# Kernel optimization log

Hardware: AMD Instinct MI355X
Metric: run time of the kernel (lower is better)

Reference implementation:

```python
import jax, jax.numpy as jnp
import numpy as np

# SLAYER neuron / simulation hyperparameters (from network.yaml)
THETA = 10.0      # spike threshold
TAU_SR = 10.0     # SRM (PSP) kernel time constant [ms]
TAU_REF = 1.0     # refractory kernel time constant [ms]
SCALE_REF = 2.0   # refractory kernel scale
TS = 1.0          # simulation step [ms]
K_SRM = 100       # truncation length of SRM kernel (eps decays ~0 by 10*tau)
K_REF = 32        # truncation length of refractory kernel (tauRef=1 -> decays fast)


def _eps_kernel(tau, k):
    # eps(t) = (t/tau) * exp(1 - t/tau), eps(0) = 0  (SLAYER SRM alpha kernel)
    t = jnp.arange(k, dtype=jnp.float32) * TS
    return (t / tau) * jnp.exp(1.0 - t / tau)


def psp(x, kern):
    # Causal temporal filter: y[..., t] = sum_j kern[j] * x[..., t - j]
    B, N, T = x.shape
    lhs = x.reshape(B * N, 1, T)
    rhs = kern[::-1].reshape(1, 1, -1)  # lax.conv is cross-correlation -> flip
    y = jax.lax.conv_general_dilated(
        lhs, rhs, window_strides=(1,), padding=[(kern.shape[0] - 1, 0)],
        dimension_numbers=('NCH', 'OIH', 'NCH'))
    return y.reshape(B, N, T)


def spike(u, refk):
    # Sequential thresholding with refractory feedback (SLAYER spikeFunction fwd).
    # u: [B, N, T] membrane drive. State r: future refractory contributions.
    kr = refk.shape[0]
    refk_shift = jnp.concatenate([refk[1:], jnp.zeros((1,), refk.dtype)])

    def step(r, u_t):
        m = u_t + r[..., 0]                      # membrane potential at t
        s = (m >= THETA).astype(u_t.dtype)       # hard spike
        r_next = jnp.concatenate([r[..., 1:], jnp.zeros_like(r[..., :1])], -1) \
                 + s[..., None] * refk_shift     # add refractory response
        return r_next, s

    uT = jnp.moveaxis(u, -1, 0)                  # [T, B, N]
    r0 = jnp.zeros(uT.shape[1:] + (kr,), u.dtype)
    _, sT = jax.lax.scan(step, r0, uT)
    return jnp.moveaxis(sT, 0, -1) / TS          # [B, N, T]


def setup_inputs() -> dict:
    key = jax.random.key(0)
    k1, k2, k3 = jax.random.split(key, 3)
    B, NIN, NHID, NOUT, T = 32, 2048, 512, 10, 350
    spike_input = (jax.random.uniform(k1, (B, NIN, T)) < 0.05).astype(jnp.float32)
    W1 = jax.random.normal(k2, (NHID, NIN), dtype=jnp.float32) * 0.05
    W2 = jax.random.normal(k3, (NOUT, NHID), dtype=jnp.float32) * 0.05
    return {"spike_input": spike_input, "W1": W1, "W2": W2}


def reference(spike_input, W1, W2):
    srm = _eps_kernel(TAU_SR, K_SRM)
    refk = -SCALE_REF * THETA * _eps_kernel(TAU_REF, K_REF)
    # layer 1: psp -> dense -> spike
    a1 = jnp.einsum('bnt,mn->bmt', psp(spike_input, srm), W1)
    s1 = spike(a1, refk)
    # layer 2: psp -> dense -> spike
    a2 = jnp.einsum('bnt,mn->bmt', psp(s1, srm), W2)
    s2 = spike(a2, refk)
    return s2
```

## Files before the change

kernel.cpp:

```cpp
#include <hip/hip_runtime.h>
#include <stdint.h>

static constexpr int B  = 32;
static constexpr int T  = 350;
static constexpr int NIN = 2048;
static constexpr int NH  = 512;
static constexpr int NO  = 10;
static constexpr int BT  = B * T;

static constexpr float THETA = 10.0f;
static constexpr float BETA  = 0.36787944117144233f;
static constexpr float CREF  = 54.365636569180904707f;

static constexpr size_t OFF_W1TS = 0;
static constexpr size_t OFF_MASK = 4196352;
static constexpr size_t OFF_SRM  = 7080960;
static constexpr size_t OFF_Z1   = 7081984;
static constexpr size_t OFF_A1   = 30019584;
static constexpr size_t OFF_LST  = OFF_A1;
static constexpr size_t OFF_CNT  = OFF_A1 + 4300800;
static constexpr size_t OFF_SMK  = 52957184;

static constexpr int SLICE_F = 8;
static constexpr int NSLICE  = NH / SLICE_F;
static constexpr int SLICE_STRIDE = 2049 * SLICE_F;

__global__ void __launch_bounds__(256) k_prep(const float* __restrict__ x,
                                              const float* __restrict__ W1,
                                              float* __restrict__ W1Ts,
                                              uint64_t* __restrict__ mask,
                                              float* __restrict__ srm28) {
    int bid = blockIdx.x;
    if (bid < 1024) {
        __shared__ uint64_t tb[6][64];
        int b = bid >> 5, nblk = bid & 31;
        int wv = threadIdx.x >> 6, lane = threadIdx.x & 63;
        for (int g = 0; g < 4; ++g) {
            float v[4][6];
            #pragma unroll
            for (int i = 0; i < 4; ++i) {
                int nr = wv + 4 * (4 * g + i);
                const float* xp = x + ((size_t)b * NIN + nblk * 64 + nr) * T;
                #pragma unroll
                for (int c = 0; c < 6; ++c) {
                    int t = c * 64 + lane;
                    v[i][c] = (t < T) ? xp[t] : 0.f;
                }
            }
            #pragma unroll
            for (int i = 0; i < 4; ++i) {
                int nr = wv + 4 * (4 * g + i);
                #pragma unroll
                for (int c = 0; c < 6; ++c) {
                    uint64_t mk = __ballot(v[i][c] != 0.0f);
                    if (lane == 0) tb[c][nr] = mk;
                }
            }
        }
        __syncthreads();
        static const uint64_t AM[6] = {
            0x00000000FFFFFFFFull, 0x0000FFFF0000FFFFull, 0x00FF00FF00FF00FFull,
            0x0F0F0F0F0F0F0F0Full, 0x3333333333333333ull, 0x5555555555555555ull };
        for (int c = wv; c < 6; c += 4) {
            uint64_t w = tb[c][lane];
            #pragma unroll
            for (int i = 0; i < 6; ++i) {
                int s = 32 >> i;
                uint64_t A = AM[i];
                uint64_t y = __shfl_xor((unsigned long long)w, s);
                if ((lane & s) == 0) w = (w & A)  | ((y & A) << s);
                else                 w = (w & ~A) | ((y & ~A) >> s);
            }
            int t = c * 64 + lane;
            if (t < T) mask[((size_t)b * 32 + nblk) * 352 + t] = w;
        }
    } else if (bid < 2048) {
        __shared__ float tile[32][33];
        int idx = bid - 1024;
        int n0 = (idx & 63) * 32, m0 = (idx >> 6) * 32;
        int tx = threadIdx.x & 31, ty0 = threadIdx.x >> 5;
        #pragma unroll
        for (int i = 0; i < 4; ++i) {
            int ty = ty0 + 8 * i;
            tile[ty][tx] = W1[(size_t)(m0 + ty) * NIN + n0 + tx];
        }
        __syncthreads();
        #pragma unroll
        for (int i = 0; i < 4; ++i) {
            int ty = ty0 + 8 * i;
            int n = n0 + ty, m = m0 + tx;
            W1Ts[(size_t)(m >> 3) * SLICE_STRIDE + n * SLICE_F + (m & 7)] = tile[tx][ty];
        }
    } else {
        int j = threadIdx.x;
        if (j < 192) {
            float v = 0.f;
            int i = j - 28;
            if (i >= 0 && i < 100) { float t = (float)i; v = (t * 0.1f) * expf(1.f - t * 0.1f); }
            srm28[j] = v;
        }
        for (int i = j; i < NSLICE * SLICE_F; i += 256)
            W1Ts[(size_t)(i >> 3) * SLICE_STRIDE + 2048 * SLICE_F + (i & 7)] = 0.f;
    }
}

__global__ void __launch_bounds__(64) k_decode(const uint64_t* __restrict__ mask,
                                               uint16_t* __restrict__ glst,
                                               int* __restrict__ gcnt) {
    __shared__ uint16_t lst[192];
    int t = blockIdx.x, b = blockIdx.y;
    int row = b * T + t;
    int lane = threadIdx.x;
    uint64_t w = (lane < 32) ? mask[((size_t)b * 32 + lane) * 352 + t] : 0ull;
    int cnt = __popcll(w);
    int pre = cnt;
    #pragma unroll
    for (int off = 1; off < 64; off <<= 1) {
        int v = __shfl_up(pre, off);
        if (lane >= off) pre += v;
    }
    int total = __shfl(pre, 63);
    int excl = pre - cnt;
    while (w) {
        int bit = __builtin_ctzll(w);
        w &= w - 1;
        lst[excl++] = (uint16_t)((lane << 6) + bit);
    }
    int padded = (total + 7) & ~7;
    if (lane < padded - total) lst[total + lane] = 2048;
    __syncthreads();
    uint16_t* op = glst + (size_t)row * 192;
    for (int i = lane; i < padded; i += 64) op[i] = lst[i];
    if (lane == 0) gcnt[row] = padded;
}

__global__ void __launch_bounds__(256) k_z1s(const uint16_t* __restrict__ glst,
                                             const int* __restrict__ gcnt,
                                             const float* __restrict__ W1Ts,
                                             float* __restrict__ z1) {
    __shared__ float w1s[SLICE_STRIDE];
    int s = blockIdx.x;
    int bt0 = blockIdx.y * (BT / 8);
    const float4* src = (const float4*)(W1Ts + (size_t)s * SLICE_STRIDE);
    for (int i = threadIdx.x; i < SLICE_STRIDE / 4; i += 256)
        ((float4*)w1s)[i] = src[i];
    __syncthreads();

    int q  = threadIdx.x & 1;
    int rl = threadIdx.x >> 1;
    for (int rr = rl; rr < BT / 8; rr += 128) {
        int row = bt0 + rr;
        int padded = gcnt[row];
        const ushort4* lp = (const ushort4*)(glst + (size_t)row * 192);
        float4 acc = {0, 0, 0, 0};
        for (int k = 0; k < padded; k += 8) {
            ushort4 q0 = lp[k >> 2];
            ushort4 q1 = lp[(k >> 2) + 1];
            const float* base = w1s + q * 4;
            float4 x0 = *(const float4*)(base + q0.x * SLICE_F);
            float4 x1 = *(const float4*)(base + q0.y * SLICE_F);
            float4 x2 = *(const float4*)(base + q0.z * SLICE_F);
            float4 x3 = *(const float4*)(base + q0.w * SLICE_F);
            float4 x4 = *(const float4*)(base + q1.x * SLICE_F);
            float4 x5 = *(const float4*)(base + q1.y * SLICE_F);
            float4 x6 = *(const float4*)(base + q1.z * SLICE_F);
            float4 x7 = *(const float4*)(base + q1.w * SLICE_F);
            acc.x += x0.x; acc.y += x0.y; acc.z += x0.z; acc.w += x0.w;
            acc.x += x1.x; acc.y += x1.y; acc.z += x1.z; acc.w += x1.w;
            acc.x += x2.x; acc.y += x2.y; acc.z += x2.z; acc.w += x2.w;
            acc.x += x3.x; acc.y += x3.y; acc.z += x3.z; acc.w += x3.w;
            acc.x += x4.x; acc.y += x4.y; acc.z += x4.z; acc.w += x4.w;
            acc.x += x5.x; acc.y += x5.y; acc.z += x5.z; acc.w += x5.w;
            acc.x += x6.x; acc.y += x6.y; acc.z += x6.z; acc.w += x6.w;
            acc.x += x7.x; acc.y += x7.y; acc.z += x7.z; acc.w += x7.w;
        }
        *(float4*)(z1 + (size_t)row * NH + s * SLICE_F + q * 4) = acc;
    }
}

__global__ void __launch_bounds__(64) k_fir1(const float* __restrict__ src,
                                             float* __restrict__ dst,
                                             const float* __restrict__ srm28) {
    __shared__ float tb[192];
    int b = blockIdx.x, half = blockIdx.y, tg = blockIdx.z;
    int lane = threadIdx.x;
    for (int i = lane; i < 192; i += 64) tb[i] = srm28[i];
    __syncthreads();
    int t0 = tg * 16;
    int m = half * 256 + lane * 4;
    const float* sp = src + (size_t)b * T * NH + m;

    float4 acc[16];
    #pragma unroll
    for (int r = 0; r < 16; ++r) acc[r] = make_float4(0.f, 0.f, 0.f, 0.f);

    int o_start = (99 - t0) >> 4;
    if (o_start < 0) o_start = 0;

    for (int o = o_start; o < 7; ++o) {
        float cw[31];
        int cb = 112 - 16 * o;
        #pragma unroll
        for (int k = 0; k < 31; ++k) cw[k] = tb[cb + k];
        int dd0 = o * 16;
        #pragma unroll
        for (int j = 0; j < 16; ++j) {
            int tau = t0 - 99 + dd0 + j;
            float4 v = make_float4(0.f, 0.f, 0.f, 0.f);
            if (tau >= 0 && tau < T) v = *(const float4*)(sp + (size_t)tau * NH);
            #pragma unroll
            for (int r = 0; r < 16; ++r) {
                float c = cw[r - j + 15];
                acc[r].x += c * v.x; acc[r].y += c * v.y;
                acc[r].z += c * v.z; acc[r].w += c * v.w;
            }
        }
    }
    {
        float e1 = tb[29], e2 = tb[30];
        int tau = t0 + 13;
        if (tau < T) {
            float4 v = *(const float4*)(sp + (size_t)tau * NH);
            acc[14].x += e1 * v.x; acc[14].y += e1 * v.y;
            acc[14].z += e1 * v.z; acc[14].w += e1 * v.w;
            acc[15].x += e2 * v.x; acc[15].y += e2 * v.y;
            acc[15].z += e2 * v.z; acc[15].w += e2 * v.w;
        }
        tau = t0 + 14;
        if (tau < T) {
            float4 v = *(const float4*)(sp + (size_t)tau * NH);
            acc[15].x += e1 * v.x; acc[15].y += e1 * v.y;
            acc[15].z += e1 * v.z; acc[15].w += e1 * v.w;
        }
    }
    #pragma unroll
    for (int r = 0; r < 16; ++r) {
        int t = t0 + r;
        if (t < T) *(float4*)(dst + ((size_t)b * T + t) * NH + m) = acc[r];
    }
}

__global__ void __launch_bounds__(64) k_scan1(const float* __restrict__ a1,
                                              uint64_t* __restrict__ smaskg) {
    constexpr int CT = 16;
    constexpr int NC = (T + CT - 1) / CT;
    int tid = blockIdx.x * 64 + threadIdx.x;
    int b = tid >> 9, m = tid & 511;
    int w8 = m >> 6;
    const float* up = a1 + (size_t)b * T * NH + m;
    float A = 0.f, Bs = 0.f;
    float c0[CT], c1[CT], c2[CT];
    #pragma unroll
    for (int j = 0; j < CT; ++j) c0[j] = up[(size_t)j * NH];
    #pragma unroll
    for (int j = 0; j < CT; ++j) {
        int t = CT + j;
        c1[j] = (t < T) ? up[(size_t)t * NH] : 0.f;
    }
    for (int c = 0; c < NC; ++c) {
        int t0 = c * CT;
        int nsteps = (T - t0 < CT) ? (T - t0) : CT;
        if (c + 2 < NC) {
            #pragma unroll
            for (int j = 0; j < CT; ++j) {
                int t = t0 + 2 * CT + j;
                c2[j] = (t < T) ? up[(size_t)t * NH] : 0.f;
            }
        }
        #pragma unroll
        for (int j = 0; j < CT; ++j) {
            if (j < nsteps) {
                float mem = c0[j] - CREF * Bs;
                float sp = (mem >= THETA) ? 1.0f : 0.0f;
                A = sp + BETA * A;
                Bs = BETA * (Bs + A);
                uint64_t mk = __ballot(sp != 0.0f);
                if (threadIdx.x == 0) smaskg[((size_t)b * T + t0 + j) * 8 + w8] = mk;
            }
        }
        #pragma unroll
        for (int j = 0; j < CT; ++j) { c0[j] = c1[j]; c1[j] = c2[j]; }
    }
}

__global__ void __launch_bounds__(256) k_tail(const uint64_t* __restrict__ smaskg,
                                              const float* __restrict__ W2,
                                              const float* __restrict__ srm28,
                                              float* __restrict__ out) {
    __shared__ float w2s_ab[NO * NH];
    __shared__ uint64_t smk[T * 8];
    __shared__ float tb[192];
    __shared__ float zb[350 * 11 + 16];
    int b = blockIdx.x, tid = threadIdx.x;
    for (int i = tid; i < NO * NH; i += 256) w2s_ab[i] = W2[i];
    const uint64_t* mp = smaskg + (size_t)b * T * 8;
    for (int i = tid; i < T * 8; i += 256) smk[i] = mp[i];
    if (tid < 192) tb[tid] = srm28[tid];
    __syncthreads();
    for (int i = tid; i < T * NO; i += 256) {
        int t = i / NO, o = i - t * NO;
        const float* wrow = w2s_ab + o * NH;
        float acc = 0.f;
        #pragma unroll
        for (int w8 = 0; w8 < 8; ++w8) {
            uint64_t mk = smk[t * 8 + w8];
            int base = w8 * 64;
            while (mk) {
                int bit = __builtin_ctzll(mk);
                mk &= mk - 1;
                acc += wrow[base + bit];
            }
        }
        zb[t * 11 + o] = acc;
    }
    __syncthreads();
    float* ab = w2s_ab;
    if (tid < 220) {
        int tt = tid / 10, o = tid - tt * 10;
        int t0 = tt * 16;
        float acc[16];
        #pragma unroll
        for (int r = 0; r < 16; ++r) acc[r] = 0.f;
        float c[16];
        #pragma unroll
        for (int r = 0; r < 16; ++r) c[r] = tb[r + 127];
        for (int oo = 0; oo < 8; ++oo) {
            #pragma unroll
            for (int j = 0; j < 16; ++j) {
                int dd = oo * 16 + j;
                int tau = t0 - 99 + dd;
                float v = (tau >= 0 && tau < T) ? zb[tau * 11 + o] : 0.f;
                #pragma unroll
                for (int r = 0; r < 16; ++r) acc[r] += c[r] * v;
                #pragma unroll
                for (int r = 15; r > 0; --r) c[r] = c[r - 1];
                int ci = 126 - dd;
                c[0] = tb[ci < 0 ? 0 : ci];
            }
        }
        #pragma unroll
        for (int r = 0; r < 16; ++r) {
            int t = t0 + r;
            if (t < T) ab[t * 10 + o] = acc[r];
        }
    }
    __syncthreads();
    if (tid < NO) {
        int o = tid;
        float A2 = 0.f, B2 = 0.f;
        float* op = out + ((size_t)b * NO + o) * T;
        for (int t = 0; t < T; ++t) {
            float mem = ab[t * 10 + o] - CREF * B2;
            float sp = (mem >= THETA) ? 1.0f : 0.0f;
            A2 = sp + BETA * A2;
            B2 = BETA * (B2 + A2);
            op[t] = sp;
        }
    }
}

extern "C" void kernel_launch(void* const* d_in, const int* in_sizes, int n_in,
                              void* d_out, int out_size, void* d_ws, size_t ws_size,
                              hipStream_t stream) {
    const float* x  = (const float*)d_in[0];
    const float* W1 = (const float*)d_in[1];
    const float* W2 = (const float*)d_in[2];
    char* ws = (char*)d_ws;
    float*    W1Ts   = (float*)(ws + OFF_W1TS);
    uint64_t* mask   = (uint64_t*)(ws + OFF_MASK);
    float*    srm    = (float*)(ws + OFF_SRM);
    float*    z1     = (float*)(ws + OFF_Z1);
    float*    a1     = (float*)(ws + OFF_A1);
    uint16_t* glst   = (uint16_t*)(ws + OFF_LST);
    int*      gcnt   = (int*)(ws + OFF_CNT);
    uint64_t* smaskg = (uint64_t*)(ws + OFF_SMK);
    float*    out    = (float*)d_out;

    hipLaunchKernelGGL(k_prep,   dim3(2049),      dim3(256), 0, stream, x, W1, W1Ts, mask, srm);
    hipLaunchKernelGGL(k_decode, dim3(T, B),      dim3(64),  0, stream, mask, glst, gcnt);
    hipLaunchKernelGGL(k_z1s,    dim3(NSLICE, 8), dim3(256), 0, stream, glst, gcnt, W1Ts, z1);
    hipLaunchKernelGGL(k_fir1,   dim3(B, 2, 22),  dim3(64),  0, stream, z1, a1, srm);
    hipLaunchKernelGGL(k_scan1,  dim3(256),       dim3(64),  0, stream, a1, smaskg);
    hipLaunchKernelGGL(k_tail,   dim3(B),         dim3(256), 0, stream, smaskg, W2, srm, out);
}
```

Baseline: 294.6 us.

## Fuse all stages into one persistent kernel with grid-wide atomic barriers

The six separate kernel launches become a single persistent kernel of 512 blocks. Each stage loops over its former virtual blocks and is separated from the next by a software grid barrier built on atomic counters, which are zeroed with a memset before launch. The goal is to remove per-launch overhead and the gaps between kernels. In exchange, occupancy is fixed at 2 blocks per CU, a 64KB shared buffer limits residency, stages with little parallelism such as the tail (32 blocks) leave most of the grid idle, and the barrier deadlocks if the 512 blocks cannot all be resident at once.

```diff
diff --git a/kernel.cpp b/kernel.cpp
--- a/kernel.cpp
+++ b/kernel.cpp
@@ -7,6 +7,8 @@
 static constexpr int NH  = 512;
 static constexpr int NO  = 10;
 static constexpr int BT  = B * T;
+
+static constexpr int GRID = 512;
 
 static constexpr float THETA = 10.0f;
 static constexpr float BETA  = 0.36787944117144233f;
@@ -20,341 +22,379 @@
 static constexpr size_t OFF_LST  = OFF_A1;
 static constexpr size_t OFF_CNT  = OFF_A1 + 4300800;
 static constexpr size_t OFF_SMK  = 52957184;
+static constexpr size_t OFF_BAR  = 53673984;
 
 static constexpr int SLICE_F = 8;
 static constexpr int NSLICE  = NH / SLICE_F;
 static constexpr int SLICE_STRIDE = 2049 * SLICE_F;
 
-__global__ void __launch_bounds__(256) k_prep(const float* __restrict__ x,
-                                              const float* __restrict__ W1,
-                                              float* __restrict__ W1Ts,
-                                              uint64_t* __restrict__ mask,
-                                              float* __restrict__ srm28) {
+__device__ __forceinline__ void gbar(int* cnt, int idx) {
+    __syncthreads();
+    __threadfence();
+    if (threadIdx.x == 0) {
+        atomicAdd(cnt + idx, 1);
+        while (__hip_atomic_load(cnt + idx, __ATOMIC_ACQUIRE,
+                                 __HIP_MEMORY_SCOPE_AGENT) < GRID) {
+            __builtin_amdgcn_s_sleep(1);
+        }
+    }
+    __syncthreads();
+    __threadfence();
+}
+
+__global__ void __launch_bounds__(256, 2) k_all(const float* __restrict__ x,
+                                                const float* __restrict__ W1,
+                                                const float* __restrict__ W2,
+                                                float* __restrict__ W1Ts,
+                                                uint64_t* __restrict__ mask,
+                                                float* __restrict__ srm28,
+                                                uint16_t* glst,
+                                                int* __restrict__ gcnt,
+                                                float* __restrict__ z1,
+                                                float* a1,
+                                                uint64_t* __restrict__ smaskg,
+                                                int* __restrict__ bar,
+                                                float* __restrict__ out) {
+    __shared__ __align__(16) char smem[65568];
     int bid = blockIdx.x;
-    if (bid < 1024) {
-        __shared__ uint64_t tb[6][64];
-        int b = bid >> 5, nblk = bid & 31;
-        int wv = threadIdx.x >> 6, lane = threadIdx.x & 63;
-        for (int g = 0; g < 4; ++g) {
-            float v[4][6];
+    int tid = threadIdx.x;
+
+    for (int vb = bid; vb < 2049; vb += GRID) {
+        if (vb < 1024) {
+            uint64_t (*tb)[64] = (uint64_t(*)[64])smem;
+            int b = vb >> 5, nblk = vb & 31;
+            int wv = tid >> 6, lane = tid & 63;
+            for (int g = 0; g < 4; ++g) {
+                float v[4][6];
+                #pragma unroll
+                for (int i = 0; i < 4; ++i) {
+                    int nr = wv + 4 * (4 * g + i);
+                    const float* xp = x + ((size_t)b * NIN + nblk * 64 + nr) * T;
+                    #pragma unroll
+                    for (int c = 0; c < 6; ++c) {
+                        int t = c * 64 + lane;
+                        v[i][c] = (t < T) ? xp[t] : 0.f;
+                    }
+                }
+                #pragma unroll
+                for (int i = 0; i < 4; ++i) {
+                    int nr = wv + 4 * (4 * g + i);
+                    #pragma unroll
+                    for (int c = 0; c < 6; ++c) {
+                        uint64_t mk = __ballot(v[i][c] != 0.0f);
+                        if (lane == 0) tb[c][nr] = mk;
+                    }
+                }
+            }
+            __syncthreads();
+            static const uint64_t AM[6] = {
+                0x00000000FFFFFFFFull, 0x0000FFFF0000FFFFull, 0x00FF00FF00FF00FFull,
+                0x0F0F0F0F0F0F0F0Full, 0x3333333333333333ull, 0x5555555555555555ull };
+            for (int c = wv; c < 6; c += 4) {
+                uint64_t w = tb[c][lane];
+                #pragma unroll
+                for (int i = 0; i < 6; ++i) {
+                    int s = 32 >> i;
+                    uint64_t A = AM[i];
+                    uint64_t y = __shfl_xor((unsigned long long)w, s);
+                    if ((lane & s) == 0) w = (w & A)  | ((y & A) << s);
+                    else                 w = (w & ~A) | ((y & ~A) >> s);
+                }
+                int t = c * 64 + lane;
+                if (t < T) mask[((size_t)b * 32 + nblk) * 352 + t] = w;
+            }
+        } else if (vb < 2048) {
+            float (*tile)[33] = (float(*)[33])smem;
+            int idx = vb - 1024;
+            int n0 = (idx & 63) * 32, m0 = (idx >> 6) * 32;
+            int tx = tid & 31, ty0 = tid >> 5;
             #pragma unroll
             for (int i = 0; i < 4; ++i) {
-                int nr = wv + 4 * (4 * g + i);
-                const float* xp = x + ((size_t)b * NIN + nblk * 64 + nr) * T;
-                #pragma unroll
-                for (int c = 0; c < 6; ++c) {
-                    int t = c * 64 + lane;
-                    v[i][c] = (t < T) ? xp[t] : 0.f;
-                }
-            }
+                int ty = ty0 + 8 * i;
+                tile[ty][tx] = W1[(size_t)(m0 + ty) * NIN + n0 + tx];
+            }
+            __syncthreads();
             #pragma unroll
             for (int i = 0; i < 4; ++i) {
-                int nr = wv + 4 * (4 * g + i);
-                #pragma unroll
-                for (int c = 0; c < 6; ++c) {
-                    uint64_t mk = __ballot(v[i][c] != 0.0f);
-                    if (lane == 0) tb[c][nr] = mk;
-                }
-            }
-        }
-        __syncthreads();
-        static const uint64_t AM[6] = {
-            0x00000000FFFFFFFFull, 0x0000FFFF0000FFFFull, 0x00FF00FF00FF00FFull,
-            0x0F0F0F0F0F0F0F0Full, 0x3333333333333333ull, 0x5555555555555555ull };
-        for (int c = wv; c < 6; c += 4) {
-            uint64_t w = tb[c][lane];
-            #pragma unroll
-            for (int i = 0; i < 6; ++i) {
-                int s = 32 >> i;
-                uint64_t A = AM[i];
-                uint64_t y = __shfl_xor((unsigned long long)w, s);
-                if ((lane & s) == 0) w = (w & A)  | ((y & A) << s);
-                else                 w = (w & ~A) | ((y & ~A) >> s);
-            }
-            int t = c * 64 + lane;
-            if (t < T) mask[((size_t)b * 32 + nblk) * 352 + t] = w;
-        }
-    } else if (bid < 2048) {
-        __shared__ float tile[32][33];
-        int idx = bid - 1024;
-        int n0 = (idx & 63) * 32, m0 = (idx >> 6) * 32;
-        int tx = threadIdx.x & 31, ty0 = threadIdx.x >> 5;
-        #pragma unroll
-        for (int i = 0; i < 4; ++i) {
-            int ty = ty0 + 8 * i;
-            tile[ty][tx] = W1[(size_t)(m0 + ty) * NIN + n0 + tx];
-        }
-        __syncthreads();
-        #pragma unroll
-        for (int i = 0; i < 4; ++i) {
-            int ty = ty0 + 8 * i;
-            int n = n0 + ty, m = m0 + tx;
-            W1Ts[(size_t)(m >> 3) * SLICE_STRIDE + n * SLICE_F + (m & 7)] = tile[tx][ty];
-        }
-    } else {
-        int j = threadIdx.x;
-        if (j < 192) {
-            float v = 0.f;
-            int i = j - 28;
-            if (i >= 0 && i < 100) { float t = (float)i; v = (t * 0.1f) * expf(1.f - t * 0.1f); }
-            srm28[j] = v;
-        }
-        for (int i = j; i < NSLICE * SLICE_F; i += 256)
-            W1Ts[(size_t)(i >> 3) * SLICE_STRIDE + 2048 * SLICE_F + (i & 7)] = 0.f;
-    }
-}
-
-__global__ void __launch_bounds__(64) k_decode(const uint64_t* __restrict__ mask,
-                                               uint16_t* __restrict__ glst,
-                                               int* __restrict__ gcnt) {
-    __shared__ uint16_t lst[192];
-    int t = blockIdx.x, b = blockIdx.y;
-    int row = b * T + t;
-    int lane = threadIdx.x;
-    uint64_t w = (lane < 32) ? mask[((size_t)b * 32 + lane) * 352 + t] : 0ull;
-    int cnt = __popcll(w);
-    int pre = cnt;
-    #pragma unroll
-    for (int off = 1; off < 64; off <<= 1) {
-        int v = __shfl_up(pre, off);
-        if (lane >= off) pre += v;
-    }
-    int total = __shfl(pre, 63);
-    int excl = pre - cnt;
-    while (w) {
-        int bit = __builtin_ctzll(w);
-        w &= w - 1;
-        lst[excl++] = (uint16_t)((lane << 6) + bit);
-    }
-    int padded = (total + 7) & ~7;
-    if (lane < padded - total) lst[total + lane] = 2048;
-    __syncthreads();
-    uint16_t* op = glst + (size_t)row * 192;
-    for (int i = lane; i < padded; i += 64) op[i] = lst[i];
-    if (lane == 0) gcnt[row] = padded;
-}
-
-__global__ void __launch_bounds__(256) k_z1s(const uint16_t* __restrict__ glst,
-                                             const int* __restrict__ gcnt,
-                                             const float* __restrict__ W1Ts,
-                                             float* __restrict__ z1) {
-    __shared__ float w1s[SLICE_STRIDE];
-    int s = blockIdx.x;
-    int bt0 = blockIdx.y * (BT / 8);
-    const float4* src = (const float4*)(W1Ts + (size_t)s * SLICE_STRIDE);
-    for (int i = threadIdx.x; i < SLICE_STRIDE / 4; i += 256)
-        ((float4*)w1s)[i] = src[i];
-    __syncthreads();
-
-    int q  = threadIdx.x & 1;
-    int rl = threadIdx.x >> 1;
-    for (int rr = rl; rr < BT / 8; rr += 128) {
-        int row = bt0 + rr;
-        int padded = gcnt[row];
-        const ushort4* lp = (const ushort4*)(glst + (size_t)row * 192);
-        float4 acc = {0, 0, 0, 0};
-        for (int k = 0; k < padded; k += 8) {
-            ushort4 q0 = lp[k >> 2];
-            ushort4 q1 = lp[(k >> 2) + 1];
-            const float* base = w1s + q * 4;
-            float4 x0 = *(const float4*)(base + q0.x * SLICE_F);
-            float4 x1 = *(const float4*)(base + q0.y * SLICE_F);
-            float4 x2 = *(const float4*)(base + q0.z * SLICE_F);
-            float4 x3 = *(const float4*)(base + q0.w * SLICE_F);
-            float4 x4 = *(const float4*)(base + q1.x * SLICE_F);
-            float4 x5 = *(const float4*)(base + q1.y * SLICE_F);
-            float4 x6 = *(const float4*)(base + q1.z * SLICE_F);
-            float4 x7 = *(const float4*)(base + q1.w * SLICE_F);
-            acc.x += x0.x; acc.y += x0.y; acc.z += x0.z; acc.w += x0.w;
-            acc.x += x1.x; acc.y += x1.y; acc.z += x1.z; acc.w += x1.w;
-            acc.x += x2.x; acc.y += x2.y; acc.z += x2.z; acc.w += x2.w;
-            acc.x += x3.x; acc.y += x3.y; acc.z += x3.z; acc.w += x3.w;
-            acc.x += x4.x; acc.y += x4.y; acc.z += x4.z; acc.w += x4.w;
-            acc.x += x5.x; acc.y += x5.y; acc.z += x5.z; acc.w += x5.w;
-            acc.x += x6.x; acc.y += x6.y; acc.z += x6.z; acc.w += x6.w;
-            acc.x += x7.x; acc.y += x7.y; acc.z += x7.z; acc.w += x7.w;
-        }
-        *(float4*)(z1 + (size_t)row * NH + s * SLICE_F + q * 4) = acc;
-    }
-}
-
-__global__ void __launch_bounds__(64) k_fir1(const float* __restrict__ src,
-                                             float* __restrict__ dst,
-                                             const float* __restrict__ srm28) {
-    __shared__ float tb[192];
-    int b = blockIdx.x, half = blockIdx.y, tg = blockIdx.z;
-    int lane = threadIdx.x;
-    for (int i = lane; i < 192; i += 64) tb[i] = srm28[i];
-    __syncthreads();
-    int t0 = tg * 16;
-    int m = half * 256 + lane * 4;
-    const float* sp = src + (size_t)b * T * NH + m;
-
-    float4 acc[16];
-    #pragma unroll
-    for (int r = 0; r < 16; ++r) acc[r] = make_float4(0.f, 0.f, 0.f, 0.f);
-
-    int o_start = (99 - t0) >> 4;
-    if (o_start < 0) o_start = 0;
-
-    for (int o = o_start; o < 7; ++o) {
-        float cw[31];
-        int cb = 112 - 16 * o;
-        #pragma unroll
-        for (int k = 0; k < 31; ++k) cw[k] = tb[cb + k];
-        int dd0 = o * 16;
-        #pragma unroll
-        for (int j = 0; j < 16; ++j) {
-            int tau = t0 - 99 + dd0 + j;
-            float4 v = make_float4(0.f, 0.f, 0.f, 0.f);
-            if (tau >= 0 && tau < T) v = *(const float4*)(sp + (size_t)tau * NH);
+                int ty = ty0 + 8 * i;
+                int n = n0 + ty, m = m0 + tx;
+                W1Ts[(size_t)(m >> 3) * SLICE_STRIDE + n * SLICE_F + (m & 7)] = tile[tx][ty];
+            }
+        } else {
+            int j = tid;
+            if (j < 192) {
+                float v = 0.f;
+                int i = j - 28;
+                if (i >= 0 && i < 100) { float t = (float)i; v = (t * 0.1f) * expf(1.f - t * 0.1f); }
+                srm28[j] = v;
+            }
+            for (int i = j; i < NSLICE * SLICE_F; i += 256)
+                W1Ts[(size_t)(i >> 3) * SLICE_STRIDE + 2048 * SLICE_F + (i & 7)] = 0.f;
+        }
+        __syncthreads();
+    }
+    gbar(bar, 0);
+
+    {
+        int w = tid >> 6, lane = tid & 63;
+        uint16_t* lst = (uint16_t*)smem + w * 200;
+        int vw = bid * 4 + w;
+        for (int k = 0; k < 6; ++k) {
+            int row = vw + 2048 * k;
+            bool act = (row < BT);
+            int padded = 0;
+            if (act) {
+                int b = row / T, t = row - b * T;
+                uint64_t wd = (lane < 32) ? mask[((size_t)b * 32 + lane) * 352 + t] : 0ull;
+                int cnt = __popcll(wd);
+                int pre = cnt;
+                #pragma unroll
+                for (int off = 1; off < 64; off <<= 1) {
+                    int v = __shfl_up(pre, off);
+                    if (lane >= off) pre += v;
+                }
+                int total = __shfl(pre, 63);
+                int excl = pre - cnt;
+                while (wd) {
+                    int bit = __builtin_ctzll(wd);
+                    wd &= wd - 1;
+                    lst[excl++] = (uint16_t)((lane << 6) + bit);
+                }
+                padded = (total + 7) & ~7;
+                if (lane < padded - total) lst[total + lane] = 2048;
+            }
+            __syncthreads();
+            if (act) {
+                uint16_t* op = glst + (size_t)row * 192;
+                for (int i = lane; i < padded; i += 64) op[i] = lst[i];
+                if (lane == 0) gcnt[row] = padded;
+            }
+            __syncthreads();
+        }
+    }
+    gbar(bar, 1);
+
+    {
+        float* w1s = (float*)smem;
+        int s = bid & 63;
+        int bt0 = (bid >> 6) * (BT / 8);
+        const float4* src = (const float4*)(W1Ts + (size_t)s * SLICE_STRIDE);
+        for (int i = tid; i < SLICE_STRIDE / 4; i += 256)
+            ((float4*)w1s)[i] = src[i];
+        __syncthreads();
+
+        int q  = tid & 1;
+        int rl = tid >> 1;
+        for (int rr = rl; rr < BT / 8; rr += 128) {
+            int row = bt0 + rr;
+            int padded = gcnt[row];
+            const ushort4* lp = (const ushort4*)(glst + (size_t)row * 192);
+            float4 acc = {0, 0, 0, 0};
+            for (int k = 0; k < padded; k += 8) {
+                ushort4 q0 = lp[k >> 2];
+                ushort4 q1 = lp[(k >> 2) + 1];
+                const float* base = w1s + q * 4;
+                float4 x0 = *(const float4*)(base + q0.x * SLICE_F);
+                float4 x1 = *(const float4*)(base + q0.y * SLICE_F);
+                float4 x2 = *(const float4*)(base + q0.z * SLICE_F);
+                float4 x3 = *(const float4*)(base + q0.w * SLICE_F);
+                float4 x4 = *(const float4*)(base + q1.x * SLICE_F);
+                float4 x5 = *(const float4*)(base + q1.y * SLICE_F);
+                float4 x6 = *(const float4*)(base + q1.z * SLICE_F);
+                float4 x7 = *(const float4*)(base + q1.w * SLICE_F);
+                acc.x += x0.x; acc.y += x0.y; acc.z += x0.z; acc.w += x0.w;
+                acc.x += x1.x; acc.y += x1.y; acc.z += x1.z; acc.w += x1.w;
+                acc.x += x2.x; acc.y += x2.y; acc.z += x2.z; acc.w += x2.w;
+                acc.x += x3.x; acc.y += x3.y; acc.z += x3.z; acc.w += x3.w;
+                acc.x += x4.x; acc.y += x4.y; acc.z += x4.z; acc.w += x4.w;
+                acc.x += x5.x; acc.y += x5.y; acc.z += x5.z; acc.w += x5.w;
+                acc.x += x6.x; acc.y += x6.y; acc.z += x6.z; acc.w += x6.w;
+                acc.x += x7.x; acc.y += x7.y; acc.z += x7.z; acc.w += x7.w;
+            }
+            *(float4*)(z1 + (size_t)row * NH + s * SLICE_F + q * 4) = acc;
+        }
+    }
+    gbar(bar, 2);
+
+    {
+        float* tbf = (float*)smem;
+        for (int i = tid; i < 192; i += 256) tbf[i] = srm28[i];
+        __syncthreads();
+        int w = tid >> 6, lane = tid & 63;
+        int vw = bid * 4 + w;
+        if (vw < 1408) {
+            int b = vw & 31, half = (vw >> 5) & 1, tg = vw >> 6;
+            int t0 = tg * 16;
+            int m = half * 256 + lane * 4;
+            const float* sp = z1 + (size_t)b * T * NH + m;
+
+            float4 acc[16];
+            #pragma unroll
+            for (int r = 0; r < 16; ++r) acc[r] = make_float4(0.f, 0.f, 0.f, 0.f);
+
+            int o_start = (99 - t0) >> 4;
+            if (o_start < 0) o_start = 0;
+
+            for (int o = o_start; o < 7; ++o) {
+                float cw[31];
+                int cb = 112 - 16 * o;
+                #pragma unroll
+                for (int kk = 0; kk < 31; ++kk) cw[kk] = tbf[cb + kk];
+                int dd0 = o * 16;
+                #pragma unroll
+                for (int j = 0; j < 16; ++j) {
+                    int tau = t0 - 99 + dd0 + j;
+                    float4 v = make_float4(0.f, 0.f, 0.f, 0.f);
+                    if (tau >= 0 && tau < T) v = *(const float4*)(sp + (size_t)tau * NH);
+                    #pragma unroll
+                    for (int r = 0; r < 16; ++r) {
+                        float c = cw[r - j + 15];
+                        acc[r].x += c * v.x; acc[r].y += c * v.y;
+                        acc[r].z += c * v.z; acc[r].w += c * v.w;
+                    }
+                }
+            }
+            {
+                float e1 = tbf[29], e2 = tbf[30];
+                int tau = t0 + 13;
+                if (tau < T) {
+                    float4 v = *(const float4*)(sp + (size_t)tau * NH);
+                    acc[14].x += e1 * v.x; acc[14].y += e1 * v.y;
+                    acc[14].z += e1 * v.z; acc[14].w += e1 * v.w;
+                    acc[15].x += e2 * v.x; acc[15].y += e2 * v.y;
+                    acc[15].z += e2 * v.z; acc[15].w += e2 * v.w;
+                }
+                tau = t0 + 14;
+                if (tau < T) {
+                    float4 v = *(const float4*)(sp + (size_t)tau * NH);
+                    acc[15].x += e1 * v.x; acc[15].y += e1 * v.y;
+                    acc[15].z += e1 * v.z; acc[15].w += e1 * v.w;
+                }
+            }
             #pragma unroll
             for (int r = 0; r < 16; ++r) {
-                float c = cw[r - j + 15];
-                acc[r].x += c * v.x; acc[r].y += c * v.y;
-                acc[r].z += c * v.z; acc[r].w += c * v.w;
-            }
-        }
-    }
+                int t = t0 + r;
+                if (t < T) *(float4*)(a1 + ((size_t)b * T + t) * NH + m) = acc[r];
+            }
+        }
+    }
+    gbar(bar, 3);
+
     {
-        float e1 = tb[29], e2 = tb[30];
-        int tau = t0 + 13;
-        if (tau < T) {
-            float4 v = *(const float4*)(sp + (size_t)tau * NH);
-            acc[14].x += e1 * v.x; acc[14].y += e1 * v.y;
-            acc[14].z += e1 * v.z; acc[14].w += e1 * v.w;
-            acc[15].x += e2 * v.x; acc[15].y += e2 * v.y;
-            acc[15].z += e2 * v.z; acc[15].w += e2 * v.w;
-        }
-        tau = t0 + 14;
-        if (tau < T) {
-            float4 v = *(const float4*)(sp + (size_t)tau * NH);
-            acc[15].x += e1 * v.x; acc[15].y += e1 * v.y;
-            acc[15].z += e1 * v.z; acc[15].w += e1 * v.w;
-        }
-    }
-    #pragma unroll
-    for (int r = 0; r < 16; ++r) {
-        int t = t0 + r;
-        if (t < T) *(float4*)(dst + ((size_t)b * T + t) * NH + m) = acc[r];
-    }
-}
-
-__global__ void __launch_bounds__(64) k_scan1(const float* __restrict__ a1,
-                                              uint64_t* __restrict__ smaskg) {
-    constexpr int CT = 16;
-    constexpr int NC = (T + CT - 1) / CT;
-    int tid = blockIdx.x * 64 + threadIdx.x;
-    int b = tid >> 9, m = tid & 511;
-    int w8 = m >> 6;
-    const float* up = a1 + (size_t)b * T * NH + m;
-    float A = 0.f, Bs = 0.f;
-    float c0[CT], c1[CT], c2[CT];
-    #pragma unroll
-    for (int j = 0; j < CT; ++j) c0[j] = up[(size_t)j * NH];
-    #pragma unroll
-    for (int j = 0; j < CT; ++j) {
-        int t = CT + j;
-        c1[j] = (t < T) ? up[(size_t)t * NH] : 0.f;
-    }
-    for (int c = 0; c < NC; ++c) {
-        int t0 = c * CT;
-        int nsteps = (T - t0 < CT) ? (T - t0) : CT;
-        if (c + 2 < NC) {
+        if ((bid & 1) == 0 && tid < 64) {
+            constexpr int CT = 16;
+            constexpr int NC = (T + CT - 1) / CT;
+            int tg = (bid >> 1) * 64 + tid;
+            int b = tg >> 9, m = tg & 511;
+            int w8 = m >> 6;
+            const float* up = a1 + (size_t)b * T * NH + m;
+            float A = 0.f, Bs = 0.f;
+            float c0[CT], c1[CT], c2[CT];
+            #pragma unroll
+            for (int j = 0; j < CT; ++j) c0[j] = up[(size_t)j * NH];
             #pragma unroll
             for (int j = 0; j < CT; ++j) {
-                int t = t0 + 2 * CT + j;
-                c2[j] = (t < T) ? up[(size_t)t * NH] : 0.f;
-            }
-        }
-        #pragma unroll
-        for (int j = 0; j < CT; ++j) {
-            if (j < nsteps) {
-                float mem = c0[j] - CREF * Bs;
+                int t = CT + j;
+                c1[j] = (t < T) ? up[(size_t)t * NH] : 0.f;
+            }
+            for (int c = 0; c < NC; ++c) {
+                int t0 = c * CT;
+                int nsteps = (T - t0 < CT) ? (T - t0) : CT;
+                if (c + 2 < NC) {
+                    #pragma unroll
+                    for (int j = 0; j < CT; ++j) {
+                        int t = t0 + 2 * CT + j;
+                        c2[j] = (t < T) ? up[(size_t)t * NH] : 0.f;
+                    }
+                }
+                #pragma unroll
+                for (int j = 0; j < CT; ++j) {
+                    if (j < nsteps) {
+                        float mem = c0[j] - CREF * Bs;
+                        float sp = (mem >= THETA) ? 1.0f : 0.0f;
+                        A = sp + BETA * A;
+                        Bs = BETA * (Bs + A);
+                        uint64_t mk = __ballot(sp != 0.0f);
+                        if (tid == 0) smaskg[((size_t)b * T + t0 + j) * 8 + w8] = mk;
+                    }
+                }
+                #pragma unroll
+                for (int j = 0; j < CT; ++j) { c0[j] = c1[j]; c1[j] = c2[j]; }
+            }
+        }
+    }
+    gbar(bar, 4);
+
+    if ((bid & 15) == 0) {
+        int b = bid >> 4;
+        float*    w2s_ab = (float*)smem;
+        uint64_t* smk    = (uint64_t*)(smem + 20480);
+        float*    tbf    = (float*)(smem + 42880);
+        float*    zb     = (float*)(smem + 43648);
+        for (int i = tid; i < NO * NH; i += 256) w2s_ab[i] = W2[i];
+        const uint64_t* mp = smaskg + (size_t)b * T * 8;
+        for (int i = tid; i < T * 8; i += 256) smk[i] = mp[i];
+        if (tid < 192) tbf[tid] = srm28[tid];
+        __syncthreads();
+        for (int i = tid; i < T * NO; i += 256) {
+            int t = i / NO, o = i - t * NO;
+            const float* wrow = w2s_ab + o * NH;
+            float acc = 0.f;
+            #pragma unroll
+            for (int w8 = 0; w8 < 8; ++w8) {
+                uint64_t mk = smk[t * 8 + w8];
+                int base = w8 * 64;
+                while (mk) {
+                    int bit = __builtin_ctzll(mk);
+                    mk &= mk - 1;
+                    acc += wrow[base + bit];
+                }
+            }
+            zb[t * 11 + o] = acc;
+        }
+        __syncthreads();
+        float* ab = w2s_ab;
+        if (tid < 220) {
+            int tt = tid / 10, o = tid - tt * 10;
+            int t0 = tt * 16;
+            float acc[16];
+            #pragma unroll
+            for (int r = 0; r < 16; ++r) acc[r] = 0.f;
+            float c[16];
+            #pragma unroll
+            for (int r = 0; r < 16; ++r) c[r] = tbf[r + 127];
+            for (int oo = 0; oo < 8; ++oo) {
+                #pragma unroll
+                for (int j = 0; j < 16; ++j) {
+                    int dd = oo * 16 + j;
+                    int tau = t0 - 99 + dd;
+                    float v = (tau >= 0 && tau < T) ? zb[tau * 11 + o] : 0.f;
+                    #pragma unroll
+                    for (int r = 0; r < 16; ++r) acc[r] += c[r] * v;
+                    #pragma unroll
+                    for (int r = 15; r > 0; --r) c[r] = c[r - 1];
+                    int ci = 126 - dd;
+                    c[0] = tbf[ci < 0 ? 0 : ci];
+                }
+            }
+            #pragma unroll
+            for (int r = 0; r < 16; ++r) {
+                int t = t0 + r;
+                if (t < T) ab[t * 10 + o] = acc[r];
+            }
+        }
+        __syncthreads();
+        if (tid < NO) {
+            int o = tid;
+            float A2 = 0.f, B2 = 0.f;
+            float* op = out + ((size_t)b * NO + o) * T;
+            for (int t = 0; t < T; ++t) {
+                float mem = ab[t * 10 + o] - CREF * B2;
                 float sp = (mem >= THETA) ? 1.0f : 0.0f;
-                A = sp + BETA * A;
-                Bs = BETA * (Bs + A);
-                uint64_t mk = __ballot(sp != 0.0f);
-                if (threadIdx.x == 0) smaskg[((size_t)b * T + t0 + j) * 8 + w8] = mk;
-            }
-        }
-        #pragma unroll
-        for (int j = 0; j < CT; ++j) { c0[j] = c1[j]; c1[j] = c2[j]; }
-    }
-}
-
-__global__ void __launch_bounds__(256) k_tail(const uint64_t* __restrict__ smaskg,
-                                              const float* __restrict__ W2,
-                                              const float* __restrict__ srm28,
-                                              float* __restrict__ out) {
-    __shared__ float w2s_ab[NO * NH];
-    __shared__ uint64_t smk[T * 8];
-    __shared__ float tb[192];
-    __shared__ float zb[350 * 11 + 16];
-    int b = blockIdx.x, tid = threadIdx.x;
-    for (int i = tid; i < NO * NH; i += 256) w2s_ab[i] = W2[i];
-    const uint64_t* mp = smaskg + (size_t)b * T * 8;
-    for (int i = tid; i < T * 8; i += 256) smk[i] = mp[i];
-    if (tid < 192) tb[tid] = srm28[tid];
-    __syncthreads();
-    for (int i = tid; i < T * NO; i += 256) {
-        int t = i / NO, o = i - t * NO;
-        const float* wrow = w2s_ab + o * NH;
-        float acc = 0.f;
-        #pragma unroll
-        for (int w8 = 0; w8 < 8; ++w8) {
-            uint64_t mk = smk[t * 8 + w8];
-            int base = w8 * 64;
-            while (mk) {
-                int bit = __builtin_ctzll(mk);
-                mk &= mk - 1;
-                acc += wrow[base + bit];
-            }
-        }
-        zb[t * 11 + o] = acc;
-    }
-    __syncthreads();
-    float* ab = w2s_ab;
-    if (tid < 220) {
-        int tt = tid / 10, o = tid - tt * 10;
-        int t0 = tt * 16;
-        float acc[16];
-        #pragma unroll
-        for (int r = 0; r < 16; ++r) acc[r] = 0.f;
-        float c[16];
-        #pragma unroll
-        for (int r = 0; r < 16; ++r) c[r] = tb[r + 127];
-        for (int oo = 0; oo < 8; ++oo) {
-            #pragma unroll
-            for (int j = 0; j < 16; ++j) {
-                int dd = oo * 16 + j;
-                int tau = t0 - 99 + dd;
-                float v = (tau >= 0 && tau < T) ? zb[tau * 11 + o] : 0.f;
-                #pragma unroll
-                for (int r = 0; r < 16; ++r) acc[r] += c[r] * v;
-                #pragma unroll
-                for (int r = 15; r > 0; --r) c[r] = c[r - 1];
-                int ci = 126 - dd;
-                c[0] = tb[ci < 0 ? 0 : ci];
-            }
-        }
-        #pragma unroll
-        for (int r = 0; r < 16; ++r) {
-            int t = t0 + r;
-            if (t < T) ab[t * 10 + o] = acc[r];
-        }
-    }
-    __syncthreads();
-    if (tid < NO) {
-        int o = tid;
-        float A2 = 0.f, B2 = 0.f;
-        float* op = out + ((size_t)b * NO + o) * T;
-        for (int t = 0; t < T; ++t) {
-            float mem = ab[t * 10 + o] - CREF * B2;
-            float sp = (mem >= THETA) ? 1.0f : 0.0f;
-            A2 = sp + BETA * A2;
-            B2 = BETA * (B2 + A2);
-            op[t] = sp;
+                A2 = sp + BETA * A2;
+                B2 = BETA * (B2 + A2);
+                op[t] = sp;
+            }
         }
     }
 }
@@ -374,12 +414,11 @@
     uint16_t* glst   = (uint16_t*)(ws + OFF_LST);
     int*      gcnt   = (int*)(ws + OFF_CNT);
     uint64_t* smaskg = (uint64_t*)(ws + OFF_SMK);
+    int*      bar    = (int*)(ws + OFF_BAR);
     float*    out    = (float*)d_out;
 
-    hipLaunchKernelGGL(k_prep,   dim3(2049),      dim3(256), 0, stream, x, W1, W1Ts, mask, srm);
-    hipLaunchKernelGGL(k_decode, dim3(T, B),      dim3(64),  0, stream, mask, glst, gcnt);
-    hipLaunchKernelGGL(k_z1s,    dim3(NSLICE, 8), dim3(256), 0, stream, glst, gcnt, W1Ts, z1);
-    hipLaunchKernelGGL(k_fir1,   dim3(B, 2, 22),  dim3(64),  0, stream, z1, a1, srm);
-    hipLaunchKernelGGL(k_scan1,  dim3(256),       dim3(64),  0, stream, a1, smaskg);
-    hipLaunchKernelGGL(k_tail,   dim3(B),         dim3(256), 0, stream, smaskg, W2, srm, out);
+    hipMemsetAsync(bar, 0, 64, stream);
+    hipLaunchKernelGGL(k_all, dim3(GRID), dim3(256), 0, stream,
+                       x, W1, W2, W1Ts, mask, srm, glst, gcnt, z1, a1,
+                       smaskg, bar, out);
 }
```

New measurement: 1.093 ms. +270.9%, slower.
